# Kernel optimization log

Measured on AMD Instinct MI355X. Metric: run time of the kernel, lower is better.

Reference implementation:

```python
import jax, jax.numpy as jnp
import numpy as np

N = 100000          # nodes
E = 1600000         # edges (avg degree 16)
IN_CH = 128
HEADS = 4
OUT_CH = 16
NEG_SLOPE = 0.2
EPS = 1e-16


def setup_inputs() -> dict:
    key = jax.random.key(0)
    k_x, k_e, k_w, k_a = jax.random.split(key, 4)
    x = jax.random.normal(k_x, (N, IN_CH), dtype=jnp.float32)
    edge_index = jax.random.randint(k_e, (2, E), 0, N, dtype=jnp.int64)
    # xavier-uniform-ish init
    lim_w = float(np.sqrt(6.0 / (IN_CH + HEADS * OUT_CH)))
    W_node = jax.random.uniform(k_w, (IN_CH, HEADS * OUT_CH), dtype=jnp.float32,
                                minval=-lim_w, maxval=lim_w)
    lim_a = float(np.sqrt(6.0 / (1 + HEADS * OUT_CH)))
    att = jax.random.uniform(k_a, (1, HEADS, OUT_CH), dtype=jnp.float32,
                             minval=-lim_a, maxval=lim_a)
    return {"x": x, "edge_index": edge_index, "W_node": W_node, "att": att}


def reference(x, edge_index, W_node, att):
    n = x.shape[0]
    h, c = att.shape[1], att.shape[2]
    # node projection: [N, H, C]
    x_proj = (x @ W_node).reshape(n, h, c)
    row, col = edge_index[0], edge_index[1]
    x_i = x_proj[row]                      # [E, H, C] source-side gather
    x_j = x_proj[col]                      # [E, H, C] dest-side gather
    a_in = jax.nn.leaky_relu(x_i + x_j, negative_slope=NEG_SLOPE)
    alpha = jnp.sum(a_in * att, axis=-1)   # [E, H] raw logits
    # segment softmax over edges grouped by destination node (col)
    seg_max = jax.ops.segment_max(alpha, col, num_segments=n)   # [N, H]
    ex = jnp.exp(alpha - seg_max[col])
    seg_sum = jax.ops.segment_sum(ex, col, num_segments=n)      # [N, H]
    alpha = ex / (seg_sum[col] + EPS)
    # weighted scatter-add aggregation
    out = jax.ops.segment_sum(x_j * alpha[..., None], col, num_segments=n)  # [N, H, C]
    # concat=False -> mean over heads
    return out.mean(axis=1)                # [N, C]
```

## Files before the change

kernel.cpp:

```cpp
#include <hip/hip_runtime.h>

#define IN_CH 128
#define NHC   64
#define OUT_C 16


__global__ void init_kernel(const int* __restrict__ ei, int* __restrict__ flags,
                            int* __restrict__ mode, int n_nodes) {
    int i = blockIdx.x * blockDim.x + threadIdx.x;
    if (i < n_nodes) flags[i] = 0;
    if (blockIdx.x == 0) {
        __shared__ int s_mode;
        if (threadIdx.x == 0) s_mode = 0;
        __syncthreads();
        int v = ei[2 * threadIdx.x + 1];
        if (v != 0) atomicOr(&s_mode, 1);
        __syncthreads();
        if (threadIdx.x == 0) *mode = s_mode;
    }
}

__global__ void flag_kernel(const int* __restrict__ ei, const int* __restrict__ mode,
                            int* __restrict__ flags, int E, int n_nodes) {
    int e = blockIdx.x * blockDim.x + threadIdx.x;
    if (e >= E) return;
    int m = *mode;
    int c = m ? ei[E + e]
              : ei[2 * E + 2 * e];
    if ((unsigned)c < (unsigned)n_nodes) flags[c] = 1;
}

__global__ __launch_bounds__(256) void flag_kernel4(
    const int* __restrict__ ei, const int* __restrict__ mode,
    int* __restrict__ flags, int E, int n_nodes) {
    int e0 = (blockIdx.x * blockDim.x + threadIdx.x) * 4;
    if (e0 >= E) return;
    int m = *mode;
    int c0, c1, c2, c3;
    if (m) {
        int4 v = *(const int4*)(ei + E + e0);
        c0 = v.x; c1 = v.y; c2 = v.z; c3 = v.w;
    } else {
        int4 a = *(const int4*)(ei + 2 * E + 2 * e0);
        int4 b = *(const int4*)(ei + 2 * E + 2 * e0 + 4);
        c0 = a.x; c1 = a.z; c2 = b.x; c3 = b.z;
    }
    if ((unsigned)c0 < (unsigned)n_nodes) flags[c0] = 1;
    if ((unsigned)c1 < (unsigned)n_nodes) flags[c1] = 1;
    if ((unsigned)c2 < (unsigned)n_nodes) flags[c2] = 1;
    if ((unsigned)c3 < (unsigned)n_nodes) flags[c3] = 1;
}

__global__ __launch_bounds__(256) void out_kernel(
    const float* __restrict__ x,
    const float* __restrict__ W,
    const int* __restrict__ flags,
    float* __restrict__ out,
    int n_nodes)
{
    __shared__ alignas(16) float wlds[IN_CH * OUT_C];
    const int tid = threadIdx.x;

    for (int i = tid; i < IN_CH * OUT_C; i += 256) {
        int k = i >> 4, c = i & 15;
        const float* wr = W + k * NHC + c;
        wlds[i] = 0.25f * (wr[0] + wr[16] + wr[32] + wr[48]);
    }
    __syncthreads();

    const int g = tid >> 2;
    const int q = tid & 3;
    const int base = blockIdx.x * 256 + g;
    const int last = n_nodes - 1;

    const int n0 = min(base,       last);
    const int n1 = min(base + 64,  last);
    const int n2 = min(base + 128, last);
    const int n3 = min(base + 192, last);

    const float4* x4 = (const float4*)x;
    const float4* w4 = (const float4*)wlds;
    const size_t b0 = (size_t)n0 * (IN_CH / 4);
    const size_t b1 = (size_t)n1 * (IN_CH / 4);
    const size_t b2 = (size_t)n2 * (IN_CH / 4);
    const size_t b3 = (size_t)n3 * (IN_CH / 4);

    float4 a0 = make_float4(0.f, 0.f, 0.f, 0.f);
    float4 a1 = make_float4(0.f, 0.f, 0.f, 0.f);
    float4 a2 = make_float4(0.f, 0.f, 0.f, 0.f);
    float4 a3 = make_float4(0.f, 0.f, 0.f, 0.f);

    #pragma unroll 2
    for (int kk = 0; kk < IN_CH / 4; ++kk) {
        float4 v0 = x4[b0 + kk];
        float4 v1 = x4[b1 + kk];
        float4 v2 = x4[b2 + kk];
        float4 v3 = x4[b3 + kk];
        float f0[4] = {v0.x, v0.y, v0.z, v0.w};
        float f1[4] = {v1.x, v1.y, v1.z, v1.w};
        float f2[4] = {v2.x, v2.y, v2.z, v2.w};
        float f3[4] = {v3.x, v3.y, v3.z, v3.w};
        #pragma unroll
        for (int i = 0; i < 4; ++i) {
            float4 w = w4[(kk * 4 + i) * 4 + q];
            a0.x += f0[i] * w.x; a0.y += f0[i] * w.y; a0.z += f0[i] * w.z; a0.w += f0[i] * w.w;
            a1.x += f1[i] * w.x; a1.y += f1[i] * w.y; a1.z += f1[i] * w.z; a1.w += f1[i] * w.w;
            a2.x += f2[i] * w.x; a2.y += f2[i] * w.y; a2.z += f2[i] * w.z; a2.w += f2[i] * w.w;
            a3.x += f3[i] * w.x; a3.y += f3[i] * w.y; a3.z += f3[i] * w.z; a3.w += f3[i] * w.w;
        }
    }

    float4* o4 = (float4*)out;
    if (base < n_nodes) {
        float s = flags[n0] ? 1.0f : 0.0f;
        o4[(size_t)n0 * 4 + q] = make_float4(a0.x * s, a0.y * s, a0.z * s, a0.w * s);
    }
    if (base + 64 < n_nodes) {
        float s = flags[n1] ? 1.0f : 0.0f;
        o4[(size_t)n1 * 4 + q] = make_float4(a1.x * s, a1.y * s, a1.z * s, a1.w * s);
    }
    if (base + 128 < n_nodes) {
        float s = flags[n2] ? 1.0f : 0.0f;
        o4[(size_t)n2 * 4 + q] = make_float4(a2.x * s, a2.y * s, a2.z * s, a2.w * s);
    }
    if (base + 192 < n_nodes) {
        float s = flags[n3] ? 1.0f : 0.0f;
        o4[(size_t)n3 * 4 + q] = make_float4(a3.x * s, a3.y * s, a3.z * s, a3.w * s);
    }
}

extern "C" void kernel_launch(void* const* d_in, const int* in_sizes, int n_in,
                              void* d_out, int out_size, void* d_ws, size_t ws_size,
                              hipStream_t stream) {
    const float* x        = (const float*)d_in[0];
    const int*   ei       = (const int*)d_in[1];
    const float* W        = (const float*)d_in[2];

    const int E       = in_sizes[1] / 2;
    const int n_nodes = in_sizes[0] / IN_CH;

    int* flags = (int*)d_ws;
    int* mode  = (int*)((char*)d_ws + (1 << 20));

    init_kernel<<<dim3((n_nodes + 255) / 256), dim3(256), 0, stream>>>(ei, flags, mode, n_nodes);
    if ((E & 3) == 0) {
        flag_kernel4<<<dim3((E / 4 + 255) / 256), dim3(256), 0, stream>>>(ei, mode, flags, E, n_nodes);
    } else {
        flag_kernel<<<dim3((E + 255) / 256), dim3(256), 0, stream>>>(ei, mode, flags, E, n_nodes);
    }
    out_kernel<<<dim3((n_nodes + 255) / 256), dim3(256), 0, stream>>>(
        x, W, flags, (float*)d_out, n_nodes);
}
```

Before: 114.6 us.

## Replace scattered global flag writes with per-block LDS bitmaps merged in projection

Destination-node flags are now built as a 100k-bit bitmap in shared memory, using LDS atomicOr in each of 256 persistent blocks. Each block writes its bitmap to its own global slot, and the projection kernel ORs the 256 slots for the words it needs. This removes 1.6M random global stores and the full flag zeroing pass. The cost is a few MB of extra slot traffic and more reads per output block. The projection kernel also drops from four to two nodes per thread and launches twice as many blocks.

```diff
diff --git a/kernel.cpp b/kernel.cpp
--- a/kernel.cpp
+++ b/kernel.cpp
@@ -4,11 +4,15 @@
 #define NHC   64
 #define OUT_C 16
 
+#define BM_WORDS 3328
+#define NSLOTS   256
+#define MODE_OFF (1 << 22)
+
 
 __global__ void init_kernel(const int* __restrict__ ei, int* __restrict__ flags,
-                            int* __restrict__ mode, int n_nodes) {
+                            int* __restrict__ mode, int n_nodes, int zero_flags) {
     int i = blockIdx.x * blockDim.x + threadIdx.x;
-    if (i < n_nodes) flags[i] = 0;
+    if (zero_flags && i < n_nodes) flags[i] = 0;
     if (blockIdx.x == 0) {
         __shared__ int s_mode;
         if (threadIdx.x == 0) s_mode = 0;
@@ -20,47 +24,68 @@
     }
 }
 
+__global__ __launch_bounds__(1024) void flag_bitmap_kernel(
+    const int* __restrict__ ei, const int* __restrict__ mode,
+    unsigned* __restrict__ slots, int E, int n_nodes)
+{
+    __shared__ alignas(16) unsigned bm[BM_WORDS];
+    const int tid = threadIdx.x;
+    for (int i = tid; i < BM_WORDS; i += 1024) bm[i] = 0u;
+    __syncthreads();
+
+    const int m = *mode;
+    const int Q = E >> 2;
+    const int gstride = gridDim.x * 1024;
+    for (int qi = blockIdx.x * 1024 + tid; qi < Q; qi += gstride) {
+        const int e0 = qi * 4;
+        int c0, c1, c2, c3;
+        if (m) {
+            int4 v = *(const int4*)(ei + E + e0);
+            c0 = v.x; c1 = v.y; c2 = v.z; c3 = v.w;
+        } else {
+            int4 a = *(const int4*)(ei + 2 * E + 2 * e0);
+            int4 b = *(const int4*)(ei + 2 * E + 2 * e0 + 4);
+            c0 = a.x; c1 = a.z; c2 = b.x; c3 = b.z;
+        }
+        if ((unsigned)c0 < (unsigned)n_nodes) atomicOr(&bm[c0 >> 5], 1u << (c0 & 31));
+        if ((unsigned)c1 < (unsigned)n_nodes) atomicOr(&bm[c1 >> 5], 1u << (c1 & 31));
+        if ((unsigned)c2 < (unsigned)n_nodes) atomicOr(&bm[c2 >> 5], 1u << (c2 & 31));
+        if ((unsigned)c3 < (unsigned)n_nodes) atomicOr(&bm[c3 >> 5], 1u << (c3 & 31));
+    }
+    if (blockIdx.x == 0 && tid < (E & 3)) {
+        const int e = (E & ~3) + tid;
+        const int c = m ? ei[E + e] : ei[2 * E + 2 * e];
+        if ((unsigned)c < (unsigned)n_nodes) atomicOr(&bm[c >> 5], 1u << (c & 31));
+    }
+    __syncthreads();
+
+    uint4* dst = (uint4*)(slots + (size_t)blockIdx.x * BM_WORDS);
+    const uint4* src = (const uint4*)bm;
+    for (int i = tid; i < BM_WORDS / 4; i += 1024) dst[i] = src[i];
+}
+
 __global__ void flag_kernel(const int* __restrict__ ei, const int* __restrict__ mode,
                             int* __restrict__ flags, int E, int n_nodes) {
     int e = blockIdx.x * blockDim.x + threadIdx.x;
     if (e >= E) return;
     int m = *mode;
-    int c = m ? ei[E + e]
-              : ei[2 * E + 2 * e];
+    int c = m ? ei[E + e] : ei[2 * E + 2 * e];
     if ((unsigned)c < (unsigned)n_nodes) flags[c] = 1;
-}
-
-__global__ __launch_bounds__(256) void flag_kernel4(
-    const int* __restrict__ ei, const int* __restrict__ mode,
-    int* __restrict__ flags, int E, int n_nodes) {
-    int e0 = (blockIdx.x * blockDim.x + threadIdx.x) * 4;
-    if (e0 >= E) return;
-    int m = *mode;
-    int c0, c1, c2, c3;
-    if (m) {
-        int4 v = *(const int4*)(ei + E + e0);
-        c0 = v.x; c1 = v.y; c2 = v.z; c3 = v.w;
-    } else {
-        int4 a = *(const int4*)(ei + 2 * E + 2 * e0);
-        int4 b = *(const int4*)(ei + 2 * E + 2 * e0 + 4);
-        c0 = a.x; c1 = a.z; c2 = b.x; c3 = b.z;
-    }
-    if ((unsigned)c0 < (unsigned)n_nodes) flags[c0] = 1;
-    if ((unsigned)c1 < (unsigned)n_nodes) flags[c1] = 1;
-    if ((unsigned)c2 < (unsigned)n_nodes) flags[c2] = 1;
-    if ((unsigned)c3 < (unsigned)n_nodes) flags[c3] = 1;
 }
 
 __global__ __launch_bounds__(256) void out_kernel(
     const float* __restrict__ x,
     const float* __restrict__ W,
+    const unsigned* __restrict__ slots,
     const int* __restrict__ flags,
     float* __restrict__ out,
-    int n_nodes)
+    int n_nodes, int use_bitmap)
 {
     __shared__ alignas(16) float wlds[IN_CH * OUT_C];
+    __shared__ unsigned s_flag[4];
     const int tid = threadIdx.x;
 
+    if (tid < 4) s_flag[tid] = 0u;
     for (int i = tid; i < IN_CH * OUT_C; i += 256) {
         int k = i >> 4, c = i & 15;
         const float* wr = W + k * NHC + c;
@@ -68,86 +93,86 @@
     }
     __syncthreads();
 
+    if (use_bitmap) {
+        const int w = tid & 3;
+        const int bw = blockIdx.x * 4 + w;
+        unsigned v = 0u;
+        #pragma unroll
+        for (int s = tid >> 2; s < NSLOTS; s += 64)
+            v |= slots[(size_t)s * BM_WORDS + bw];
+        if (v) atomicOr(&s_flag[w], v);
+        __syncthreads();
+    }
+
     const int g = tid >> 2;
     const int q = tid & 3;
-    const int base = blockIdx.x * 256 + g;
+    const int n0 = blockIdx.x * 128 + g;
+    const int n1 = n0 + 64;
     const int last = n_nodes - 1;
-
-    const int n0 = min(base,       last);
-    const int n1 = min(base + 64,  last);
-    const int n2 = min(base + 128, last);
-    const int n3 = min(base + 192, last);
+    const int m0 = min(n0, last);
+    const int m1 = min(n1, last);
 
     const float4* x4 = (const float4*)x;
     const float4* w4 = (const float4*)wlds;
-    const size_t b0 = (size_t)n0 * (IN_CH / 4);
-    const size_t b1 = (size_t)n1 * (IN_CH / 4);
-    const size_t b2 = (size_t)n2 * (IN_CH / 4);
-    const size_t b3 = (size_t)n3 * (IN_CH / 4);
+    const size_t b0 = (size_t)m0 * (IN_CH / 4);
+    const size_t b1 = (size_t)m1 * (IN_CH / 4);
 
     float4 a0 = make_float4(0.f, 0.f, 0.f, 0.f);
     float4 a1 = make_float4(0.f, 0.f, 0.f, 0.f);
-    float4 a2 = make_float4(0.f, 0.f, 0.f, 0.f);
-    float4 a3 = make_float4(0.f, 0.f, 0.f, 0.f);
 
-    #pragma unroll 2
+    #pragma unroll 4
     for (int kk = 0; kk < IN_CH / 4; ++kk) {
         float4 v0 = x4[b0 + kk];
         float4 v1 = x4[b1 + kk];
-        float4 v2 = x4[b2 + kk];
-        float4 v3 = x4[b3 + kk];
         float f0[4] = {v0.x, v0.y, v0.z, v0.w};
         float f1[4] = {v1.x, v1.y, v1.z, v1.w};
-        float f2[4] = {v2.x, v2.y, v2.z, v2.w};
-        float f3[4] = {v3.x, v3.y, v3.z, v3.w};
         #pragma unroll
         for (int i = 0; i < 4; ++i) {
             float4 w = w4[(kk * 4 + i) * 4 + q];
             a0.x += f0[i] * w.x; a0.y += f0[i] * w.y; a0.z += f0[i] * w.z; a0.w += f0[i] * w.w;
             a1.x += f1[i] * w.x; a1.y += f1[i] * w.y; a1.z += f1[i] * w.z; a1.w += f1[i] * w.w;
-            a2.x += f2[i] * w.x; a2.y += f2[i] * w.y; a2.z += f2[i] * w.z; a2.w += f2[i] * w.w;
-            a3.x += f3[i] * w.x; a3.y += f3[i] * w.y; a3.z += f3[i] * w.z; a3.w += f3[i] * w.w;
         }
     }
 
+    float s0, s1;
+    if (use_bitmap) {
+        s0 = ((s_flag[g >> 5]       >> (g & 31)) & 1u) ? 1.0f : 0.0f;
+        s1 = ((s_flag[(g >> 5) + 2] >> (g & 31)) & 1u) ? 1.0f : 0.0f;
+    } else {
+        s0 = flags[m0] ? 1.0f : 0.0f;
+        s1 = flags[m1] ? 1.0f : 0.0f;
+    }
+
     float4* o4 = (float4*)out;
-    if (base < n_nodes) {
-        float s = flags[n0] ? 1.0f : 0.0f;
-        o4[(size_t)n0 * 4 + q] = make_float4(a0.x * s, a0.y * s, a0.z * s, a0.w * s);
-    }
-    if (base + 64 < n_nodes) {
-        float s = flags[n1] ? 1.0f : 0.0f;
-        o4[(size_t)n1 * 4 + q] = make_float4(a1.x * s, a1.y * s, a1.z * s, a1.w * s);
-    }
-    if (base + 128 < n_nodes) {
-        float s = flags[n2] ? 1.0f : 0.0f;
-        o4[(size_t)n2 * 4 + q] = make_float4(a2.x * s, a2.y * s, a2.z * s, a2.w * s);
-    }
-    if (base + 192 < n_nodes) {
-        float s = flags[n3] ? 1.0f : 0.0f;
-        o4[(size_t)n3 * 4 + q] = make_float4(a3.x * s, a3.y * s, a3.z * s, a3.w * s);
-    }
+    if (n0 < n_nodes)
+        o4[(size_t)n0 * 4 + q] = make_float4(a0.x * s0, a0.y * s0, a0.z * s0, a0.w * s0);
+    if (n1 < n_nodes)
+        o4[(size_t)n1 * 4 + q] = make_float4(a1.x * s1, a1.y * s1, a1.z * s1, a1.w * s1);
 }
 
 extern "C" void kernel_launch(void* const* d_in, const int* in_sizes, int n_in,
                               void* d_out, int out_size, void* d_ws, size_t ws_size,
                               hipStream_t stream) {
-    const float* x        = (const float*)d_in[0];
-    const int*   ei       = (const int*)d_in[1];
-    const float* W        = (const float*)d_in[2];
+    const float* x  = (const float*)d_in[0];
+    const int*   ei = (const int*)d_in[1];
+    const float* W  = (const float*)d_in[2];
 
     const int E       = in_sizes[1] / 2;
     const int n_nodes = in_sizes[0] / IN_CH;
 
+    unsigned* slots = (unsigned*)d_ws;
     int* flags = (int*)d_ws;
-    int* mode  = (int*)((char*)d_ws + (1 << 20));
+    int* mode  = (int*)((char*)d_ws + MODE_OFF);
 
-    init_kernel<<<dim3((n_nodes + 255) / 256), dim3(256), 0, stream>>>(ei, flags, mode, n_nodes);
-    if ((E & 3) == 0) {
-        flag_kernel4<<<dim3((E / 4 + 255) / 256), dim3(256), 0, stream>>>(ei, mode, flags, E, n_nodes);
+    const int use_bitmap = (n_nodes <= BM_WORDS * 32) ? 1 : 0;
+
+    if (use_bitmap) {
+        init_kernel<<<dim3(1), dim3(256), 0, stream>>>(ei, flags, mode, n_nodes, 0);
+        flag_bitmap_kernel<<<dim3(NSLOTS), dim3(1024), 0, stream>>>(ei, mode, slots, E, n_nodes);
     } else {
+        init_kernel<<<dim3((n_nodes + 255) / 256), dim3(256), 0, stream>>>(ei, flags, mode, n_nodes, 1);
         flag_kernel<<<dim3((E + 255) / 256), dim3(256), 0, stream>>>(ei, mode, flags, E, n_nodes);
     }
-    out_kernel<<<dim3((n_nodes + 255) / 256), dim3(256), 0, stream>>>(
-        x, W, flags, (float*)d_out, n_nodes);
+    out_kernel<<<dim3((n_nodes + 127) / 128), dim3(256), 0, stream>>>(
+        x, W, slots, flags, (float*)d_out, n_nodes, use_bitmap);
 }
```

After: 115.8 us. About the same (+1.1%).
